# Optimization experiments

Measured on AMD Instinct MI355X. Metric: run time of the kernel, lower is better.

Reference implementation:

```python
import jax, jax.numpy as jnp
import numpy as np

EPS = 1e-12


def setup_inputs() -> dict:
    key = jax.random.key(0)
    x = jax.random.normal(key, (32, 3000, 512), dtype=jnp.float32)
    return {"x": x, "kernel_size": 100}


def _window_sum(a, k):
    # sliding sum of length-k windows (stride 1) along axis 1; a: [B, Tpad, D] -> [B, Tpad-k+1, D]
    return jax.lax.reduce_window(a, 0.0, jax.lax.add, (1, k, 1), (1, 1, 1), 'VALID')


def reference(x, kernel_size):
    k = int(kernel_size)
    B, T, D = x.shape
    if T < k:
        # global CMVN fallback (torch.std default is unbiased, ddof=1)
        m = x.mean(axis=1, keepdims=True)
        v = x.std(axis=1, ddof=1, keepdims=True)
        return (x - m) / (v + EPS)
    # per-position effective window counts matching torch's denom construction:
    # ramp k//2..k-1, then k for the interior, then k-1 down to k//2
    denom = jnp.concatenate([
        jnp.arange(k // 2, k),
        jnp.full((T - k,), k),
        jnp.arange(k - 1, k // 2 - 1, -1),
    ]).astype(x.dtype)[None, :, None]  # [1, T, 1]
    # zero-pad time axis exactly like F.pad(..., (k//2, k//2 - 1))
    x_pad = jnp.pad(x, ((0, 0), (k // 2, k // 2 - 1), (0, 0)))
    s1 = _window_sum(x_pad, k)            # sum of window values (zeros at pads) [B, T, D]
    s2 = _window_sum(x_pad * x_pad, k)    # sum of squares                        [B, T, D]
    m = s1 / denom
    # torch sums (window - m)^2 over all k slots INCLUDING zero-padded slots:
    # sum (w - m)^2 = s2 - 2*m*s1 + k*m^2
    var_sum = s2 - 2.0 * m * s1 + k * m * m
    v = jnp.sqrt(var_sum / (k - 1))
    return (x - m) / (v + EPS)
```

## Files before the change

kernel.cpp:

```cpp
#include <hip/hip_runtime.h>

#define EPS 1e-12f


typedef float f4 __attribute__((ext_vector_type(4)));

constexpr int Bq = 32, Tq = 3000, Dq = 512;
constexpr int SEG = 25;
constexpr int NSEG = Tq / SEG;
constexpr int NCHUNK = Tq / SEG;
constexpr int NB = Bq * NCHUNK;
constexpr int NXCD = 8;

__global__ __launch_bounds__(128) void seg_sums_kernel(
    const float* __restrict__ x, float* __restrict__ ws)
{
    const int s = blockIdx.x;
    const int b = blockIdx.y;
    const int d4 = threadIdx.x;
    const float* xp = x + ((size_t)b * Tq) * Dq + (size_t)d4 * 4;

    f4 a1 = {0.f, 0.f, 0.f, 0.f};
    f4 a2 = a1, b1 = a1, b2 = a1;
    const int r0 = s * SEG;
#pragma unroll 5
    for (int j = 0; j < SEG; j += 2) {
        const f4 v = *(const f4*)(xp + (size_t)(r0 + j) * Dq);
        a1 += v; a2 += v * v;
        if (j + 1 < SEG) {
            const f4 w = *(const f4*)(xp + (size_t)(r0 + j + 1) * Dq);
            b1 += w; b2 += w * w;
        }
    }
    f4* w1 = (f4*)ws;
    f4* w2 = w1 + (size_t)Bq * NSEG * (Dq / 4);
    const size_t idx = ((size_t)b * NSEG + s) * (Dq / 4) + d4;
    w1[idx] = a1 + b1;
    w2[idx] = a2 + b2;
}

__global__ __launch_bounds__(128) void mavn_kernel(
    const float* __restrict__ x, const int* __restrict__ kptr,
    float* __restrict__ out, const float* __restrict__ ws, int use_seg)
{
    const int g = blockIdx.x;
    const int xcd = g & (NXCD - 1);
    const int slot = g >> 3;
    const int pair = xcd * (NB / NXCD) + slot;
    const int b = pair / NCHUNK;
    const int c = pair % NCHUNK;
    const int t0 = c * SEG;
    const int t1 = t0 + SEG;

    const int k = kptr[0];
    const int half = k >> 1;
    const int d4 = threadIdx.x;
    const size_t base = ((size_t)b * Tq) * (size_t)Dq + (size_t)d4 * 4;
    const float* xp = x + base;
    float* op = out + base;

    f4 s1 = {0.f, 0.f, 0.f, 0.f};
    f4 s2 = s1;

    const bool seg_ok = use_seg && (k == 4 * SEG);

    if (seg_ok) {
        const f4* w1 = (const f4*)ws;
        const f4* w2 = w1 + (size_t)Bq * NSEG * (Dq / 4);
        const int slo = (c - 2 < 0) ? 0 : c - 2;
        const int shi = (c + 2 > NSEG) ? NSEG : c + 2;
        for (int s = slo; s < shi; ++s) {
            const size_t idx = ((size_t)b * NSEG + s) * (Dq / 4) + d4;
            s1 += w1[idx];
            s2 += w2[idx];
        }
    } else {
        const int wlo = t0 - half;
        const int whi = t0 + (k - half);
        for (int j = (wlo > 0 ? wlo : 0); j < (whi < Tq ? whi : Tq); ++j) {
            const f4 v = *(const f4*)(xp + (size_t)j * Dq);
            s1 += v; s2 += v * v;
        }
    }

    const float kf = (float)k;
    const float inv_km1 = 1.0f / (float)(k - 1);
    const int tail_start = Tq - (k - half);

    const bool interior = seg_ok && (t0 >= half) &&
                          (t0 + SEG + (k - half) - 1 <= Tq - 1) &&
                          (t0 + SEG - 1 < tail_start);

    if (interior) {
        const float inv_k = 1.0f / kf;
        {
            const f4 xc = *(const f4*)(xp + (size_t)t0 * Dq);
            f4 o;
#pragma unroll
            for (int cc = 0; cc < 4; ++cc) {
                const float m = s1[cc] * inv_k;
                float var_sum = s2[cc] - m * s1[cc];
                var_sum = fmaxf(var_sum, 1e-12f);
                const float r = __builtin_amdgcn_rsqf(var_sum * inv_km1);
                o[cc] = (xc[cc] - m) * r;
            }
            __builtin_nontemporal_store(o, (f4*)(op + (size_t)t0 * Dq));
        }
        f4 nx = *(const f4*)(xp + (size_t)(t0 + 1) * Dq);
        f4 ia = *(const f4*)(xp + (size_t)(t0 + (k - half)) * Dq);
        f4 ob = *(const f4*)(xp + (size_t)(t0 - half) * Dq);
        for (int j = 1; j < SEG; ++j) {
            const f4 cnum = nx;
            const f4 cin = ia;
            const f4 cob = ob;
            {
                const int jn = (j + 1 < SEG) ? j + 1 : j;
                nx = *(const f4*)(xp + (size_t)(t0 + jn) * Dq);
                ia = *(const f4*)(xp + (size_t)(t0 + jn + (k - half) - 1) * Dq);
                ob = *(const f4*)(xp + (size_t)(t0 + jn - half - 1) * Dq);
            }
            s1 += cin - cob;
            s2 += cin * cin - cob * cob;
            f4 o;
#pragma unroll
            for (int cc = 0; cc < 4; ++cc) {
                const float m = s1[cc] * inv_k;
                float var_sum = s2[cc] - m * s1[cc];
                var_sum = fmaxf(var_sum, 1e-12f);
                const float r = __builtin_amdgcn_rsqf(var_sum * inv_km1);
                o[cc] = (cnum[cc] - m) * r;
            }
            __builtin_nontemporal_store(o, (f4*)(op + (size_t)(t0 + j) * Dq));
        }
        return;
    }

    f4 nx = *(const f4*)(xp + (size_t)t0 * Dq);
    f4 ia = {0.f, 0.f, 0.f, 0.f};
    f4 ob = ia;
    float wa = 0.f, wb = 0.f;

    for (int t = t0; t < t1; ++t) {
        const f4 cnum = nx;
        const f4 cin = ia;
        const f4 cout = ob;
        const float cwa = wa, cwb = wb;

        {
            const int tn = (t + 1 < t1) ? t + 1 : t;
            nx = *(const f4*)(xp + (size_t)tn * Dq);
            int ja = tn + (k - half) - 1;
            int jr = tn - half - 1;
            wa = (ja < Tq && tn > t0) ? 1.f : 0.f;
            wb = (jr >= 0 && tn > t0) ? 1.f : 0.f;
            ja = ja < Tq - 1 ? ja : Tq - 1; ja = ja > 0 ? ja : 0;
            jr = jr > 0 ? jr : 0;
            ia = *(const f4*)(xp + (size_t)ja * Dq);
            ob = *(const f4*)(xp + (size_t)jr * Dq);
        }

        s1 += cwa * cin - cwb * cout;
        s2 += cwa * cin * cin - cwb * cout * cout;

        int idn = half + t;
        idn = idn < k ? idn : k;
        const int tail = (k - 1) - (t - tail_start);
        idn = idn < tail ? idn : tail;
        const float inv_denom = __builtin_amdgcn_rcpf((float)idn);

        f4 o;
#pragma unroll
        for (int cc = 0; cc < 4; ++cc) {
            const float m = s1[cc] * inv_denom;
            float var_sum = s2[cc] - 2.0f * m * s1[cc] + kf * m * m;
            var_sum = fmaxf(var_sum, 0.0f);
            const float sd = __builtin_amdgcn_sqrtf(var_sum * inv_km1);
            o[cc] = (cnum[cc] - m) * __builtin_amdgcn_rcpf(sd + EPS);
        }
        __builtin_nontemporal_store(o, (f4*)(op + (size_t)t * Dq));
    }
}

extern "C" void kernel_launch(void* const* d_in, const int* in_sizes, int n_in,
                              void* d_out, int out_size, void* d_ws, size_t ws_size,
                              hipStream_t stream) {
    const float* x = (const float*)d_in[0];
    const int* kptr = (const int*)d_in[1];
    float* out = (float*)d_out;
    (void)in_sizes; (void)n_in; (void)out_size;

    const size_t ws_need = 2ull * Bq * NSEG * Dq * sizeof(float);
    const int use_seg = (d_ws != nullptr && ws_size >= ws_need) ? 1 : 0;

    if (use_seg) {
        dim3 g1(NSEG, Bq);
        seg_sums_kernel<<<g1, 128, 0, stream>>>(x, (float*)d_ws);
    }
    mavn_kernel<<<NB, 128, 0, stream>>>(x, kptr, out, (const float*)d_ws, use_seg);
}
```

Baseline: 98.81 us.

## Drop segment-sum pre-pass, use longer chunks with direct window init

```diff
diff --git a/kernel.cpp b/kernel.cpp
--- a/kernel.cpp
+++ b/kernel.cpp
@@ -6,42 +6,14 @@
 typedef float f4 __attribute__((ext_vector_type(4)));
 
 constexpr int Bq = 32, Tq = 3000, Dq = 512;
-constexpr int SEG = 25;
-constexpr int NSEG = Tq / SEG;
+constexpr int SEG = 75;
 constexpr int NCHUNK = Tq / SEG;
 constexpr int NB = Bq * NCHUNK;
 constexpr int NXCD = 8;
 
-__global__ __launch_bounds__(128) void seg_sums_kernel(
-    const float* __restrict__ x, float* __restrict__ ws)
-{
-    const int s = blockIdx.x;
-    const int b = blockIdx.y;
-    const int d4 = threadIdx.x;
-    const float* xp = x + ((size_t)b * Tq) * Dq + (size_t)d4 * 4;
-
-    f4 a1 = {0.f, 0.f, 0.f, 0.f};
-    f4 a2 = a1, b1 = a1, b2 = a1;
-    const int r0 = s * SEG;
-#pragma unroll 5
-    for (int j = 0; j < SEG; j += 2) {
-        const f4 v = *(const f4*)(xp + (size_t)(r0 + j) * Dq);
-        a1 += v; a2 += v * v;
-        if (j + 1 < SEG) {
-            const f4 w = *(const f4*)(xp + (size_t)(r0 + j + 1) * Dq);
-            b1 += w; b2 += w * w;
-        }
-    }
-    f4* w1 = (f4*)ws;
-    f4* w2 = w1 + (size_t)Bq * NSEG * (Dq / 4);
-    const size_t idx = ((size_t)b * NSEG + s) * (Dq / 4) + d4;
-    w1[idx] = a1 + b1;
-    w2[idx] = a2 + b2;
-}
-
 __global__ __launch_bounds__(128) void mavn_kernel(
     const float* __restrict__ x, const int* __restrict__ kptr,
-    float* __restrict__ out, const float* __restrict__ ws, int use_seg)
+    float* __restrict__ out)
 {
     const int g = blockIdx.x;
     const int xcd = g & (NXCD - 1);
@@ -61,35 +33,32 @@
 
     f4 s1 = {0.f, 0.f, 0.f, 0.f};
     f4 s2 = s1;
-
-    const bool seg_ok = use_seg && (k == 4 * SEG);
-
-    if (seg_ok) {
-        const f4* w1 = (const f4*)ws;
-        const f4* w2 = w1 + (size_t)Bq * NSEG * (Dq / 4);
-        const int slo = (c - 2 < 0) ? 0 : c - 2;
-        const int shi = (c + 2 > NSEG) ? NSEG : c + 2;
-        for (int s = slo; s < shi; ++s) {
-            const size_t idx = ((size_t)b * NSEG + s) * (Dq / 4) + d4;
-            s1 += w1[idx];
-            s2 += w2[idx];
+    {
+        f4 a1 = s1, a2 = s1;
+        const int wlo = (t0 - half > 0) ? t0 - half : 0;
+        const int whi = (t0 + (k - half) < Tq) ? t0 + (k - half) : Tq;
+        int j = wlo;
+        for (; j + 1 < whi; j += 2) {
+            const f4 v = *(const f4*)(xp + (size_t)j * Dq);
+            const f4 w = *(const f4*)(xp + (size_t)(j + 1) * Dq);
+            s1 += v; s2 += v * v;
+            a1 += w; a2 += w * w;
         }
-    } else {
-        const int wlo = t0 - half;
-        const int whi = t0 + (k - half);
-        for (int j = (wlo > 0 ? wlo : 0); j < (whi < Tq ? whi : Tq); ++j) {
+        if (j < whi) {
             const f4 v = *(const f4*)(xp + (size_t)j * Dq);
             s1 += v; s2 += v * v;
         }
+        s1 += a1; s2 += a2;
     }
 
     const float kf = (float)k;
     const float inv_km1 = 1.0f / (float)(k - 1);
     const int tail_start = Tq - (k - half);
 
-    const bool interior = seg_ok && (t0 >= half) &&
-                          (t0 + SEG + (k - half) - 1 <= Tq - 1) &&
-                          (t0 + SEG - 1 < tail_start);
+    const bool interior =
+        (t0 >= half) && (t0 >= k - half) &&
+        (t1 - 1 + (k - half) - 1 <= Tq - 1) &&
+        (t1 - 1 < tail_start);
 
     if (interior) {
         const float inv_k = 1.0f / kf;
@@ -106,31 +75,49 @@
             }
             __builtin_nontemporal_store(o, (f4*)(op + (size_t)t0 * Dq));
         }
-        f4 nx = *(const f4*)(xp + (size_t)(t0 + 1) * Dq);
-        f4 ia = *(const f4*)(xp + (size_t)(t0 + (k - half)) * Dq);
-        f4 ob = *(const f4*)(xp + (size_t)(t0 - half) * Dq);
-        for (int j = 1; j < SEG; ++j) {
-            const f4 cnum = nx;
-            const f4 cin = ia;
-            const f4 cob = ob;
+        const int inoff = (k - half) - 1;
+        const int oboff = -(half + 1);
+        f4 n0 = *(const f4*)(xp + (size_t)(t0 + 1) * Dq);
+        f4 n1 = *(const f4*)(xp + (size_t)(t0 + 2) * Dq);
+        f4 i0 = *(const f4*)(xp + (size_t)(t0 + 1 + inoff) * Dq);
+        f4 i1 = *(const f4*)(xp + (size_t)(t0 + 2 + inoff) * Dq);
+        f4 o0 = *(const f4*)(xp + (size_t)(t0 + 1 + oboff) * Dq);
+        f4 o1 = *(const f4*)(xp + (size_t)(t0 + 2 + oboff) * Dq);
+        for (int j = 1; j < SEG; j += 2) {
+            const f4 cn0 = n0, cn1 = n1, ci0 = i0, ci1 = i1, co0 = o0, co1 = o1;
             {
-                const int jn = (j + 1 < SEG) ? j + 1 : j;
-                nx = *(const f4*)(xp + (size_t)(t0 + jn) * Dq);
-                ia = *(const f4*)(xp + (size_t)(t0 + jn + (k - half) - 1) * Dq);
-                ob = *(const f4*)(xp + (size_t)(t0 + jn - half - 1) * Dq);
+                const int jn = (j + 2 <= SEG - 2) ? j + 2 : j;
+                n0 = *(const f4*)(xp + (size_t)(t0 + jn) * Dq);
+                n1 = *(const f4*)(xp + (size_t)(t0 + jn + 1) * Dq);
+                i0 = *(const f4*)(xp + (size_t)(t0 + jn + inoff) * Dq);
+                i1 = *(const f4*)(xp + (size_t)(t0 + jn + 1 + inoff) * Dq);
+                o0 = *(const f4*)(xp + (size_t)(t0 + jn + oboff) * Dq);
+                o1 = *(const f4*)(xp + (size_t)(t0 + jn + 1 + oboff) * Dq);
             }
-            s1 += cin - cob;
-            s2 += cin * cin - cob * cob;
-            f4 o;
+            s1 += ci0 - co0;
+            s2 += ci0 * ci0 - co0 * co0;
+            f4 oa;
 #pragma unroll
             for (int cc = 0; cc < 4; ++cc) {
                 const float m = s1[cc] * inv_k;
                 float var_sum = s2[cc] - m * s1[cc];
                 var_sum = fmaxf(var_sum, 1e-12f);
                 const float r = __builtin_amdgcn_rsqf(var_sum * inv_km1);
-                o[cc] = (cnum[cc] - m) * r;
+                oa[cc] = (cn0[cc] - m) * r;
             }
-            __builtin_nontemporal_store(o, (f4*)(op + (size_t)(t0 + j) * Dq));
+            __builtin_nontemporal_store(oa, (f4*)(op + (size_t)(t0 + j) * Dq));
+            s1 += ci1 - co1;
+            s2 += ci1 * ci1 - co1 * co1;
+            f4 ob2;
+#pragma unroll
+            for (int cc = 0; cc < 4; ++cc) {
+                const float m = s1[cc] * inv_k;
+                float var_sum = s2[cc] - m * s1[cc];
+                var_sum = fmaxf(var_sum, 1e-12f);
+                const float r = __builtin_amdgcn_rsqf(var_sum * inv_km1);
+                ob2[cc] = (cn1[cc] - m) * r;
+            }
+            __builtin_nontemporal_store(ob2, (f4*)(op + (size_t)(t0 + j + 1) * Dq));
         }
         return;
     }
@@ -187,14 +174,7 @@
     const float* x = (const float*)d_in[0];
     const int* kptr = (const int*)d_in[1];
     float* out = (float*)d_out;
-    (void)in_sizes; (void)n_in; (void)out_size;
+    (void)in_sizes; (void)n_in; (void)out_size; (void)d_ws; (void)ws_size;
 
-    const size_t ws_need = 2ull * Bq * NSEG * Dq * sizeof(float);
-    const int use_seg = (d_ws != nullptr && ws_size >= ws_need) ? 1 : 0;
-
-    if (use_seg) {
-        dim3 g1(NSEG, Bq);
-        seg_sums_kernel<<<g1, 128, 0, stream>>>(x, (float*)d_ws);
-    }
-    mavn_kernel<<<NB, 128, 0, stream>>>(x, kptr, out, (const float*)d_ws, use_seg);
+    mavn_kernel<<<NB, 128, 0, stream>>>(x, kptr, out);
 }
```

Result: slower. 155.1 us (+56.9%).
